# Optimization experiments

Hardware: AMD Instinct MI355X
Metric: run time of the kernel (lower is better)

Reference implementation:

```python
import jax, jax.numpy as jnp
import numpy as np

B, S, HID = 1, 4096, 2048
NH, NKV, HD = 16, 4, 128
BLK, LOCAL, GLOB, STRIDE = 128, 4, 4, 8
NEG = -1e9


def _rotate_half(x):
    x1 = x[..., : x.shape[-1] // 2]
    x2 = x[..., x.shape[-1] // 2 :]
    return jnp.concatenate([-x2, x1], axis=-1)


def setup_inputs() -> dict:
    key = jax.random.key(0)
    ks = jax.random.split(key, 6)
    hidden_states = jax.random.normal(ks[0], (B, S, HID), jnp.float32)
    attention_mask_2d = jnp.ones((B, S), jnp.float32)
    # RoPE tables (b=1 broadcasts over batch, heads)
    pos = jnp.arange(S, dtype=jnp.float32)
    inv = 1.0 / (10000.0 ** (jnp.arange(0, HD, 2, dtype=jnp.float32) / HD))
    fr = pos[:, None] * inv[None, :]
    emb = jnp.concatenate([fr, fr], axis=-1)
    cos = jnp.cos(emb)[None]
    sin = jnp.sin(emb)[None]
    sc = 0.02
    Wq = jax.random.normal(ks[1], (HID, NH * HD), jnp.float32) * sc
    Wk = jax.random.normal(ks[2], (HID, NKV * HD), jnp.float32) * sc
    Wv = jax.random.normal(ks[3], (HID, NKV * HD), jnp.float32) * sc
    Wo = jax.random.normal(ks[4], (NH * HD, HID), jnp.float32) * sc
    return dict(hidden_states=hidden_states, attention_mask_2d=attention_mask_2d,
                cos=cos, sin=sin, Wq=Wq, Wk=Wk, Wv=Wv, Wo=Wo)


def reference(hidden_states, attention_mask_2d, cos, sin, Wq, Wk, Wv, Wo):
    b, Sq, _ = hidden_states.shape
    q = (hidden_states @ Wq).reshape(b, Sq, NH, HD).transpose(0, 2, 1, 3)
    k = (hidden_states @ Wk).reshape(b, Sq, NKV, HD).transpose(0, 2, 1, 3)
    v = (hidden_states @ Wv).reshape(b, Sq, NKV, HD).transpose(0, 2, 1, 3)
    c, s = cos[:, None], sin[:, None]  # broadcast over heads
    q = q * c + _rotate_half(q) * s
    k = k * c + _rotate_half(k) * s
    rep = NH // NKV
    k = jnp.repeat(k, rep, axis=1)
    v = jnp.repeat(v, rep, axis=1)

    scaling = HD ** -0.5
    N = Sq // BLK  # seq divisible by block_size -> pad=0 in the original
    qb = q.reshape(b, NH, N, BLK, HD).astype(jnp.float32)
    kb = k.reshape(b, NH, N, BLK, HD).astype(jnp.float32)
    vb = v.reshape(b, NH, N, BLK, HD).astype(jnp.float32)
    km = attention_mask_2d.reshape(b, N, BLK)

    # ---- local windows: LOCAL blocks ending at the current block ----
    Lp = LOCAL - 1
    kp = jnp.pad(kb, ((0, 0), (0, 0), (Lp, 0), (0, 0), (0, 0)))
    vp = jnp.pad(vb, ((0, 0), (0, 0), (Lp, 0), (0, 0), (0, 0)))
    kmp = jnp.pad(km, ((0, 0), (Lp, 0), (0, 0)))  # padded blocks masked (0)
    win = jnp.arange(N)[:, None] + jnp.arange(LOCAL)[None, :]  # (N, LOCAL)
    k_local = kp[:, :, win]          # (b,h,N,LOCAL,BLK,HD)
    v_local = vp[:, :, win]
    km_local = kmp[:, win]           # (b,N,LOCAL,BLK)

    s_local = jnp.einsum('bhntd,bhnlsd->bhntls', qb, k_local) * scaling
    s_local = s_local + (1.0 - km_local)[:, None, :, None, :, :] * NEG
    intra = jnp.triu(jnp.full((BLK, BLK), NEG, jnp.float32), 1)  # causal inside current block only
    s_local = s_local.at[:, :, :, :, -1, :].add(intra)
    s_local = s_local.reshape(b, NH, N, BLK, LOCAL * BLK)

    # ---- global blocks: block 0 + strided past blocks, dedup -> masked ----
    i = jnp.arange(N)
    offsets = jnp.arange(GLOB - 1, 0, -1) * STRIDE
    idx = jnp.clip(i[:, None] - offsets[None, :], 0)
    idx = jnp.concatenate([jnp.zeros((N, 1), idx.dtype), idx], axis=1)  # (N, GLOB)
    dup = idx[:, 1:] == idx[:, :-1]
    g_valid = jnp.concatenate([jnp.ones((N, 1), bool), ~dup], axis=1).astype(jnp.float32)
    k_g = kb[:, :, idx]              # (b,h,N,GLOB,BLK,HD) gather of global blocks
    v_g = vb[:, :, idx]
    km_g = km[:, idx] * g_valid[None, :, :, None]  # (b,N,GLOB,BLK)

    s_g = jnp.einsum('bhntd,bhngsd->bhntgs', qb, k_g) * scaling
    s_g = s_g + (1.0 - km_g)[:, None, :, None, :, :] * NEG
    s_g = s_g.reshape(b, NH, N, BLK, GLOB * BLK)

    scores = jnp.concatenate([s_local, s_g], axis=-1)  # (b,h,N,BLK,(LOCAL+GLOB)*BLK)
    v_all = jnp.concatenate([v_local.reshape(b, NH, N, LOCAL * BLK, HD),
                             v_g.reshape(b, NH, N, GLOB * BLK, HD)], axis=-2)
    probs = jax.nn.softmax(scores, axis=-1)  # dropout_p = 0 (eval)
    out = jnp.einsum('bhntk,bhnkd->bhntd', probs, v_all)
    out = out.reshape(b, NH, Sq, HD).transpose(0, 2, 1, 3).reshape(b, Sq, NH * HD)
    return out @ Wo
```

## Files before the change

### kernel.cpp

```cpp
#include <hip/hip_runtime.h>
#include <hip/hip_bf16.h>
#include <cstdint>

#define NEGV   (-1000000000.0f)
#define SCALE  0.08838834764831845f

typedef __bf16 bf16x8 __attribute__((ext_vector_type(8)));
typedef float  f32x4  __attribute__((ext_vector_type(4)));
typedef unsigned short u16;
typedef unsigned int   u32;

#define MFMA16(a, b, c) __builtin_amdgcn_mfma_f32_16x16x32_bf16((a), (b), (c), 0, 0, 0)

#define WS_XP    ((size_t)0)
#define WS_AOP   ((size_t)0)
#define WS_WQP   ((size_t)8388608)
#define WS_WKP   ((size_t)12582912)
#define WS_WVP   ((size_t)13631488)
#define WS_WOP   ((size_t)14680064)
#define WS_QF    ((size_t)18874368)
#define WS_KF    ((size_t)27262976)
#define WS_VF    ((size_t)29360128)

__device__ __forceinline__ u16 f2bf(float f) {
  union { float f; u32 u; } v; v.f = f;
  u32 u = v.u;
  u += 0x7FFFu + ((u >> 16) & 1u);
  return (u16)(u >> 16);
}

__device__ __forceinline__ void gl_lds16(const u16* g, u16* l) {
  __builtin_amdgcn_global_load_lds((const __attribute__((address_space(1))) u32*)g,
                                   (__attribute__((address_space(3))) u32*)l,
                                   16, 0, 0);
}

__device__ __forceinline__ int fragoff(int row, int k) {
  return ((row >> 4) * 64 + ((k >> 3) & 3) * 16 + (row & 15)) * 8 + (k & 7);
}

__global__ __launch_bounds__(256, 4)
void convert_kernel(const float* __restrict__ X,
                    const float* __restrict__ Wq,
                    const float* __restrict__ Wk,
                    const float* __restrict__ Wv,
                    const float* __restrict__ Wo,
                    u16* __restrict__ ws)
{
  const int t = blockIdx.x;
  const int tid = threadIdx.x;
  const float* src; u16* dst; int tt, ldn; bool amode = false;
  if (t < 2048)      { src = X;  dst = ws + WS_XP;  tt = t;        ldn = 2048; amode = true; }
  else if (t < 3072) { src = Wq; dst = ws + WS_WQP; tt = t - 2048; ldn = 2048; }
  else if (t < 3328) { src = Wk; dst = ws + WS_WKP; tt = t - 3072; ldn = 512;  }
  else if (t < 3584) { src = Wv; dst = ws + WS_WVP; tt = t - 3328; ldn = 512;  }
  else               { src = Wo; dst = ws + WS_WOP; tt = t - 3584; ldn = 2048; }
  const int rb = tt >> 6, kb = tt & 63;

  if (amode) {
    #pragma unroll
    for (int p = 0; p < 2; ++p) {
      const int c = tid + 256 * p;
      const int row = (c >> 6) * 16 + (c & 15);
      const int k0  = ((c >> 4) & 3) * 8;
      union { u16 h[8]; uint4 v; } pk;
      const float* s0 = src + (size_t)(rb * 128 + row) * 2048 + kb * 32 + k0;
      const float4 a0 = *reinterpret_cast<const float4*>(s0);
      const float4 a1 = *reinterpret_cast<const float4*>(s0 + 4);
      pk.h[0] = f2bf(a0.x); pk.h[1] = f2bf(a0.y); pk.h[2] = f2bf(a0.z); pk.h[3] = f2bf(a0.w);
      pk.h[4] = f2bf(a1.x); pk.h[5] = f2bf(a1.y); pk.h[6] = f2bf(a1.z); pk.h[7] = f2bf(a1.w);
      *reinterpret_cast<uint4*>(dst + (size_t)tt * 4096 + c * 8) = pk.v;
    }
  } else {
    __shared__ u16 Ls[32][136];
    #pragma unroll
    for (int i = 0; i < 4; ++i) {
      const int c = tid + 256 * i;
      const int k = c >> 5, n4 = c & 31;
      const float4 wv = *reinterpret_cast<const float4*>(
          src + (size_t)(kb * 32 + k) * ldn + rb * 128 + n4 * 4);
      u16* d = &Ls[k][n4 * 4];
      d[0] = f2bf(wv.x); d[1] = f2bf(wv.y); d[2] = f2bf(wv.z); d[3] = f2bf(wv.w);
    }
    __syncthreads();
    #pragma unroll
    for (int p = 0; p < 2; ++p) {
      const int c = tid + 256 * p;
      const int row = (c >> 6) * 16 + (c & 15);
      const int k0  = ((c >> 4) & 3) * 8;
      union { u16 h[8]; uint4 v; } pk;
      #pragma unroll
      for (int j = 0; j < 8; ++j) pk.h[j] = Ls[k0 + j][row];
      *reinterpret_cast<uint4*>(dst + (size_t)tt * 4096 + c * 8) = pk.v;
    }
  }
}

__device__ __forceinline__ void gemm_core(const u16* __restrict__ pa,
                                          const u16* __restrict__ pb,
                                          u16* As, u16* Bs,
                                          int tid, int wave, int lane,
                                          f32x4 acc[2][8])
{
  for (int it = 0; it < 64; ++it) {
    __syncthreads();
    gl_lds16(pa + tid * 8,         As + tid * 8);
    gl_lds16(pa + (tid + 256) * 8, As + (tid + 256) * 8);
    gl_lds16(pb + tid * 8,         Bs + tid * 8);
    gl_lds16(pb + (tid + 256) * 8, Bs + (tid + 256) * 8);
    pa += 4096; pb += 4096;
    __syncthreads();
    bf16x8 af0 = *reinterpret_cast<const bf16x8*>(As + (wave * 2 + 0) * 512 + lane * 8);
    bf16x8 af1 = *reinterpret_cast<const bf16x8*>(As + (wave * 2 + 1) * 512 + lane * 8);
    #pragma unroll
    for (int nt = 0; nt < 8; ++nt) {
      const bf16x8 bfr = *reinterpret_cast<const bf16x8*>(Bs + nt * 512 + lane * 8);
      acc[0][nt] = MFMA16(af0, bfr, acc[0][nt]);
      acc[1][nt] = MFMA16(af1, bfr, acc[1][nt]);
    }
  }
}

__global__ __launch_bounds__(256, 2)
void qkv_kernel(const float* __restrict__ cosp,
                const float* __restrict__ sinp,
                u16* __restrict__ ws)
{
  const int mb = blockIdx.x, bn = blockIdx.y;
  const int tid = threadIdx.x;
  const int wave = tid >> 6, lane = tid & 63;
  const int lq = lane >> 4, l16 = lane & 15;

  const u16* Ab = ws + WS_XP + (size_t)mb * 64 * 4096;
  const u16* Bb; int seg, hh;
  if (bn < 16)      { Bb = ws + WS_WQP + (size_t)bn * 64 * 4096;        seg = 0; hh = bn; }
  else if (bn < 20) { Bb = ws + WS_WKP + (size_t)(bn - 16) * 64 * 4096; seg = 1; hh = bn - 16; }
  else              { Bb = ws + WS_WVP + (size_t)(bn - 20) * 64 * 4096; seg = 2; hh = bn - 20; }

  __shared__ __align__(16) u16 As[4096];
  __shared__ __align__(16) u16 Bs[4096];

  f32x4 acc[2][8];
  #pragma unroll
  for (int i = 0; i < 2; ++i)
    #pragma unroll
    for (int j = 0; j < 8; ++j)
      #pragma unroll
      for (int r = 0; r < 4; ++r) acc[i][j][r] = 0.0f;

  gemm_core(Ab, Bb, As, Bs, tid, wave, lane, acc);

  const int m0 = mb * 128;
  if (seg == 2) {
    u16* V = ws + WS_VF + (size_t)hh * 524288;
    #pragma unroll
    for (int mt = 0; mt < 2; ++mt)
      #pragma unroll
      for (int nt = 0; nt < 8; ++nt) {
        const int d = nt * 16 + l16;
        #pragma unroll
        for (int r = 0; r < 4; ++r) {
          const int s = m0 + wave * 32 + mt * 16 + lq * 4 + r;
          V[(s >> 5) * 4096 + fragoff(d, s & 31)] = f2bf(acc[mt][nt][r]);
        }
      }
  } else {
    u16* D = ws + ((seg == 0) ? WS_QF : WS_KF) + (size_t)hh * 524288;
    #pragma unroll
    for (int mt = 0; mt < 2; ++mt)
      #pragma unroll
      for (int r = 0; r < 4; ++r) {
        const int s = m0 + wave * 32 + mt * 16 + lq * 4 + r;
        const int sl = s & 127;
        u16* Dt = D + (size_t)(s >> 7) * 16384;
        #pragma unroll
        for (int nt = 0; nt < 4; ++nt) {
          const int d1 = nt * 16 + l16, d2 = d1 + 64;
          const float c  = cosp[s * 128 + d1];
          const float sn = sinp[s * 128 + d1];
          const float v1 = acc[mt][nt][r], v2 = acc[mt][nt + 4][r];
          Dt[(d1 >> 5) * 4096 + fragoff(sl, d1 & 31)] = f2bf(v1 * c - v2 * sn);
          Dt[(d2 >> 5) * 4096 + fragoff(sl, d2 & 31)] = f2bf(v2 * c + v1 * sn);
        }
      }
  }
}

__global__ __launch_bounds__(512, 4)
void attn_kernel(const float* __restrict__ amask, u16* __restrict__ ws)
{
  const int n = blockIdx.x, h = blockIdx.y;
  const int kvh = h >> 2;
  const int tid = threadIdx.x;
  const int wave = tid >> 6, lane = tid & 63;
  const int lq = lane >> 4, l16 = lane & 15;

  const u16* Kfb = ws + WS_KF + (size_t)kvh * 524288;
  const u16* Vfb = ws + WS_VF + (size_t)kvh * 524288;
  u16* AOp = ws + WS_AOP;

  __shared__ __align__(16) u16 bufK[16384];
  __shared__ __align__(16) u16 bufV[16384];

  const u16* Qb = ws + WS_QF + (size_t)h * 524288 + (size_t)n * 16384;
  bf16x8 qf[4];
  #pragma unroll
  for (int kk = 0; kk < 4; ++kk)
    qf[kk] = *reinterpret_cast<const bf16x8*>(Qb + (size_t)kk * 4096 + (wave * 64 + lane) * 8);

  f32x4 O[8];
  #pragma unroll
  for (int j = 0; j < 8; ++j)
    #pragma unroll
    for (int r = 0; r < 4; ++r) O[j][r] = 0.0f;
  float mrow[4], lrow[4];
  #pragma unroll
  for (int r = 0; r < 4; ++r) { mrow[r] = -3.0e38f; lrow[r] = 0.0f; }

  int gidx[4]; bool gval[4];
  gidx[0] = 0;
  gidx[1] = (n - 24 > 0) ? n - 24 : 0;
  gidx[2] = (n - 16 > 0) ? n - 16 : 0;
  gidx[3] = (n - 8  > 0) ? n - 8  : 0;
  gval[0] = true;
  gval[1] = (gidx[1] != gidx[0]);
  gval[2] = (gidx[2] != gidx[1]);
  gval[3] = (gidx[3] != gidx[2]);

  for (int kb = 0; kb < 8; ++kb) {
    int bkey; bool bvalid; bool intra;
    if (kb < 4) { bkey = n - 3 + kb; bvalid = (bkey >= 0); intra = (kb == 3); }
    else        { bkey = gidx[kb - 4]; bvalid = gval[kb - 4]; intra = false; }
    if (!bvalid) continue;

    const u16* Kb = Kfb + (size_t)bkey * 16384;
    const u16* Vb = Vfb + (size_t)bkey * 16384;
    __syncthreads();
    #pragma unroll
    for (int p = 0; p < 4; ++p) {
      gl_lds16(Kb + (tid + 512 * p) * 8, bufK + (tid + 512 * p) * 8);
      gl_lds16(Vb + (tid + 512 * p) * 8, bufV + (tid + 512 * p) * 8);
    }
    __syncthreads();

    f32x4 sacc[8];
    #pragma unroll
    for (int j = 0; j < 8; ++j)
      #pragma unroll
      for (int r = 0; r < 4; ++r) sacc[j][r] = 0.0f;
    #pragma unroll
    for (int kk = 0; kk < 4; ++kk)
      #pragma unroll
      for (int nt = 0; nt < 8; ++nt) {
        const bf16x8 bfr = *reinterpret_cast<const bf16x8*>(
            bufK + ((kk * 8 + nt) * 64 + lane) * 8);
        sacc[nt] = MFMA16(qf[kk], bfr, sacc[nt]);
      }

    float kmv[8];
    #pragma unroll
    for (int nt = 0; nt < 8; ++nt)
      kmv[nt] = amask[bkey * 128 + nt * 16 + l16];

    __syncthreads();

    u16* pw = bufK + wave * 2048;
    #pragma unroll
    for (int r = 0; r < 4; ++r) {
      const int tq = wave * 16 + lq * 4 + r;
      float sv[8];
      float rmax = -3.0e38f;
      #pragma unroll
      for (int nt = 0; nt < 8; ++nt) {
        float s = sacc[nt][r] * SCALE + (1.0f - kmv[nt]) * NEGV;
        const int tk = nt * 16 + l16;
        if (intra && tk > tq) s += NEGV;
        sv[nt] = s;
        rmax = fmaxf(rmax, s);
      }
      #pragma unroll
      for (int off = 1; off < 16; off <<= 1)
        rmax = fmaxf(rmax, __shfl_xor(rmax, off, 64));
      const float mold = mrow[r];
      const float mnew = fmaxf(mold, rmax);
      const float alpha = __expf(mold - mnew);
      float rsum = 0.0f;
      u16 pb[8];
      #pragma unroll
      for (int nt = 0; nt < 8; ++nt) {
        const float pe = __expf(sv[nt] - mnew);
        rsum += pe;
        pb[nt] = f2bf(pe);
      }
      #pragma unroll
      for (int off = 1; off < 16; off <<= 1)
        rsum += __shfl_xor(rsum, off, 64);
      lrow[r] = lrow[r] * alpha + rsum;
      mrow[r] = mnew;
      #pragma unroll
      for (int nt = 0; nt < 8; ++nt) O[nt][r] *= alpha;
      #pragma unroll
      for (int nt = 0; nt < 8; ++nt)
        pw[(nt >> 1) * 512 + ((((nt & 1) * 2 + (l16 >> 3)) * 16) + lq * 4 + r) * 8 + (l16 & 7)] = pb[nt];
    }

    #pragma unroll
    for (int kk = 0; kk < 4; ++kk) {
      const bf16x8 pf = *reinterpret_cast<const bf16x8*>(pw + kk * 512 + lane * 8);
      #pragma unroll
      for (int nt = 0; nt < 8; ++nt) {
        const bf16x8 vfr = *reinterpret_cast<const bf16x8*>(
            bufV + ((kk * 8 + nt) * 64 + lane) * 8);
        O[nt] = MFMA16(pf, vfr, O[nt]);
      }
    }
  }

  #pragma unroll
  for (int r = 0; r < 4; ++r) {
    const float inv = 1.0f / lrow[r];
    const int s = n * 128 + wave * 16 + lq * 4 + r;
    #pragma unroll
    for (int nt = 0; nt < 8; ++nt) {
      const int kcol = h * 128 + nt * 16 + l16;
      AOp[((size_t)(s >> 7) * 64 + (kcol >> 5)) * 4096 + fragoff(s & 127, kcol & 31)] =
          f2bf(O[nt][r] * inv);
    }
  }
}

__global__ __launch_bounds__(256, 2)
void outproj_kernel(const u16* __restrict__ ws, float* __restrict__ Out)
{
  const int mb = blockIdx.x, bn = blockIdx.y;
  const int tid = threadIdx.x;
  const int wave = tid >> 6, lane = tid & 63;
  const int lq = lane >> 4, l16 = lane & 15;

  const u16* Ab = ws + WS_AOP + (size_t)mb * 64 * 4096;
  const u16* Bb = ws + WS_WOP + (size_t)bn * 64 * 4096;

  __shared__ __align__(16) u16 As[4096];
  __shared__ __align__(16) u16 Bs[4096];

  f32x4 acc[2][8];
  #pragma unroll
  for (int i = 0; i < 2; ++i)
    #pragma unroll
    for (int j = 0; j < 8; ++j)
      #pragma unroll
      for (int r = 0; r < 4; ++r) acc[i][j][r] = 0.0f;

  gemm_core(Ab, Bb, (u16*)As, (u16*)Bs, tid, wave, lane, acc);

  #pragma unroll
  for (int mt = 0; mt < 2; ++mt)
    #pragma unroll
    for (int nt = 0; nt < 8; ++nt) {
      const int ccol = bn * 128 + nt * 16 + l16;
      #pragma unroll
      for (int r = 0; r < 4; ++r) {
        const int s = mb * 128 + wave * 32 + mt * 16 + lq * 4 + r;
        Out[(size_t)s * 2048 + ccol] = acc[mt][nt][r];
      }
    }
}

extern "C" void kernel_launch(void* const* d_in, const int* in_sizes, int n_in,
                              void* d_out, int out_size, void* d_ws, size_t ws_size,
                              hipStream_t stream) {
  const float* X     = (const float*)d_in[0];
  const float* amask = (const float*)d_in[1];
  const float* cosp  = (const float*)d_in[2];
  const float* sinp  = (const float*)d_in[3];
  const float* Wq    = (const float*)d_in[4];
  const float* Wk    = (const float*)d_in[5];
  const float* Wv    = (const float*)d_in[6];
  const float* Wo    = (const float*)d_in[7];
  float* Out = (float*)d_out;
  u16* ws = (u16*)d_ws;

  hipLaunchKernelGGL(convert_kernel, dim3(4608), dim3(256), 0, stream,
                     X, Wq, Wk, Wv, Wo, ws);
  hipLaunchKernelGGL(qkv_kernel, dim3(32, 24), dim3(256), 0, stream,
                     cosp, sinp, ws);
  hipLaunchKernelGGL(attn_kernel, dim3(32, 16), dim3(512), 0, stream,
                     amask, ws);
  hipLaunchKernelGGL(outproj_kernel, dim3(32, 16), dim3(256), 0, stream,
                     ws, Out);
}
```

Measured before the change: 293.0 us.

## Prefetch next K/V block into registers and fold softmax scale into Q

The attention kernel now loads the next key/value block into registers while the current block is computed, staging it to LDS at the start of the next iteration. P gets its own LDS region, which removes one barrier per block. The softmax scale and log2(e) are folded into Q during the QKV epilogue so the kernel can use exp2 directly. The kernel also loops only over the valid block indices, launches as a 1D grid with the heaviest query blocks first, and uses 96KB of dynamic LDS with a lower occupancy bound. In exchange it uses more registers for the prefetch buffers and keeps fewer blocks resident per CU.

Measured after the change: 345.5 us. 1.18x slower.

```diff
diff --git a/kernel.cpp b/kernel.cpp
--- a/kernel.cpp
+++ b/kernel.cpp
@@ -4,6 +4,9 @@
 
 #define NEGV   (-1000000000.0f)
 #define SCALE  0.08838834764831845f
+#define LOG2E  1.4426950408889634f
+#define QSC    (SCALE * LOG2E)
+#define NEGL2  (NEGV * LOG2E)
 
 typedef __bf16 bf16x8 __attribute__((ext_vector_type(8)));
 typedef float  f32x4  __attribute__((ext_vector_type(4)));
@@ -166,6 +169,7 @@
       }
   } else {
     u16* D = ws + ((seg == 0) ? WS_QF : WS_KF) + (size_t)hh * 524288;
+    const float qs = (seg == 0) ? QSC : 1.0f;
     #pragma unroll
     for (int mt = 0; mt < 2; ++mt)
       #pragma unroll
@@ -179,17 +183,22 @@
           const float c  = cosp[s * 128 + d1];
           const float sn = sinp[s * 128 + d1];
           const float v1 = acc[mt][nt][r], v2 = acc[mt][nt + 4][r];
-          Dt[(d1 >> 5) * 4096 + fragoff(sl, d1 & 31)] = f2bf(v1 * c - v2 * sn);
-          Dt[(d2 >> 5) * 4096 + fragoff(sl, d2 & 31)] = f2bf(v2 * c + v1 * sn);
+          Dt[(d1 >> 5) * 4096 + fragoff(sl, d1 & 31)] = f2bf((v1 * c - v2 * sn) * qs);
+          Dt[(d2 >> 5) * 4096 + fragoff(sl, d2 & 31)] = f2bf((v2 * c + v1 * sn) * qs);
         }
       }
   }
 }
 
-__global__ __launch_bounds__(512, 4)
+__global__ __launch_bounds__(512, 2)
 void attn_kernel(const float* __restrict__ amask, u16* __restrict__ ws)
 {
-  const int n = blockIdx.x, h = blockIdx.y;
+  extern __shared__ u16 smem[];
+  u16* bufK = smem;
+  u16* bufV = smem + 16384;
+  const int bx = blockIdx.x;
+  const int n = 31 - (bx >> 4);
+  const int h = bx & 15;
   const int kvh = h >> 2;
   const int tid = threadIdx.x;
   const int wave = tid >> 6, lane = tid & 63;
@@ -198,9 +207,7 @@
   const u16* Kfb = ws + WS_KF + (size_t)kvh * 524288;
   const u16* Vfb = ws + WS_VF + (size_t)kvh * 524288;
   u16* AOp = ws + WS_AOP;
-
-  __shared__ __align__(16) u16 bufK[16384];
-  __shared__ __align__(16) u16 bufV[16384];
+  u16* Pw = smem + 32768 + wave * 2048;
 
   const u16* Qb = ws + WS_QF + (size_t)h * 524288 + (size_t)n * 16384;
   bf16x8 qf[4];
@@ -217,29 +224,52 @@
   #pragma unroll
   for (int r = 0; r < 4; ++r) { mrow[r] = -3.0e38f; lrow[r] = 0.0f; }
 
-  int gidx[4]; bool gval[4];
-  gidx[0] = 0;
-  gidx[1] = (n - 24 > 0) ? n - 24 : 0;
-  gidx[2] = (n - 16 > 0) ? n - 16 : 0;
-  gidx[3] = (n - 8  > 0) ? n - 8  : 0;
-  gval[0] = true;
-  gval[1] = (gidx[1] != gidx[0]);
-  gval[2] = (gidx[2] != gidx[1]);
-  gval[3] = (gidx[3] != gidx[2]);
-
-  for (int kb = 0; kb < 8; ++kb) {
-    int bkey; bool bvalid; bool intra;
-    if (kb < 4) { bkey = n - 3 + kb; bvalid = (bkey >= 0); intra = (kb == 3); }
-    else        { bkey = gidx[kb - 4]; bvalid = gval[kb - 4]; intra = false; }
-    if (!bvalid) continue;
-
-    const u16* Kb = Kfb + (size_t)bkey * 16384;
-    const u16* Vb = Vfb + (size_t)bkey * 16384;
+  const int L = (n < 3 ? n : 3) + 1;
+  const int G = (n >= 25) ? 3 : (n >= 17) ? 2 : (n >= 9) ? 1 : 0;
+  const int nv = L + 1 + G;
+  #define KBOF(i) ((i) < L ? n - L + 1 + (i) : ((i) == L ? 0 : n - 8 * (G - ((i) - L - 1))))
+
+  uint4 pk[4], pv[4]; float biasN[8];
+  {
+    const int b0 = KBOF(0);
+    const u16* Kb = Kfb + (size_t)b0 * 16384;
+    const u16* Vb = Vfb + (size_t)b0 * 16384;
+    #pragma unroll
+    for (int p = 0; p < 4; ++p) {
+      pk[p] = *reinterpret_cast<const uint4*>(Kb + (tid + 512 * p) * 8);
+      pv[p] = *reinterpret_cast<const uint4*>(Vb + (tid + 512 * p) * 8);
+    }
+    #pragma unroll
+    for (int nt = 0; nt < 8; ++nt)
+      biasN[nt] = (1.0f - amask[b0 * 128 + nt * 16 + l16]) * NEGL2;
+  }
+
+  #pragma unroll
+  for (int i = 0; i < 8; ++i) {
+    if (i >= nv) break;
+    const bool intra = (i == L - 1);
+
     __syncthreads();
     #pragma unroll
     for (int p = 0; p < 4; ++p) {
-      gl_lds16(Kb + (tid + 512 * p) * 8, bufK + (tid + 512 * p) * 8);
-      gl_lds16(Vb + (tid + 512 * p) * 8, bufV + (tid + 512 * p) * 8);
+      *reinterpret_cast<uint4*>(bufK + (tid + 512 * p) * 8) = pk[p];
+      *reinterpret_cast<uint4*>(bufV + (tid + 512 * p) * 8) = pv[p];
+    }
+    float biasC[8];
+    #pragma unroll
+    for (int nt = 0; nt < 8; ++nt) biasC[nt] = biasN[nt];
+    if (i + 1 < nv) {
+      const int nb = KBOF(i + 1);
+      const u16* Kb = Kfb + (size_t)nb * 16384;
+      const u16* Vb = Vfb + (size_t)nb * 16384;
+      #pragma unroll
+      for (int p = 0; p < 4; ++p) {
+        pk[p] = *reinterpret_cast<const uint4*>(Kb + (tid + 512 * p) * 8);
+        pv[p] = *reinterpret_cast<const uint4*>(Vb + (tid + 512 * p) * 8);
+      }
+      #pragma unroll
+      for (int nt = 0; nt < 8; ++nt)
+        biasN[nt] = (1.0f - amask[nb * 128 + nt * 16 + l16]) * NEGL2;
     }
     __syncthreads();
 
@@ -257,14 +287,6 @@
         sacc[nt] = MFMA16(qf[kk], bfr, sacc[nt]);
       }
 
-    float kmv[8];
-    #pragma unroll
-    for (int nt = 0; nt < 8; ++nt)
-      kmv[nt] = amask[bkey * 128 + nt * 16 + l16];
-
-    __syncthreads();
-
-    u16* pw = bufK + wave * 2048;
     #pragma unroll
     for (int r = 0; r < 4; ++r) {
       const int tq = wave * 16 + lq * 4 + r;
@@ -272,9 +294,9 @@
       float rmax = -3.0e38f;
       #pragma unroll
       for (int nt = 0; nt < 8; ++nt) {
-        float s = sacc[nt][r] * SCALE + (1.0f - kmv[nt]) * NEGV;
+        float s = sacc[nt][r] + biasC[nt];
         const int tk = nt * 16 + l16;
-        if (intra && tk > tq) s += NEGV;
+        if (intra && tk > tq) s += NEGL2;
         sv[nt] = s;
         rmax = fmaxf(rmax, s);
       }
@@ -283,12 +305,12 @@
         rmax = fmaxf(rmax, __shfl_xor(rmax, off, 64));
       const float mold = mrow[r];
       const float mnew = fmaxf(mold, rmax);
-      const float alpha = __expf(mold - mnew);
+      const float alpha = exp2f(mold - mnew);
       float rsum = 0.0f;
       u16 pb[8];
       #pragma unroll
       for (int nt = 0; nt < 8; ++nt) {
-        const float pe = __expf(sv[nt] - mnew);
+        const float pe = exp2f(sv[nt] - mnew);
         rsum += pe;
         pb[nt] = f2bf(pe);
       }
@@ -301,12 +323,12 @@
       for (int nt = 0; nt < 8; ++nt) O[nt][r] *= alpha;
       #pragma unroll
       for (int nt = 0; nt < 8; ++nt)
-        pw[(nt >> 1) * 512 + ((((nt & 1) * 2 + (l16 >> 3)) * 16) + lq * 4 + r) * 8 + (l16 & 7)] = pb[nt];
+        Pw[(nt >> 1) * 512 + ((((nt & 1) * 2 + (l16 >> 3)) * 16) + lq * 4 + r) * 8 + (l16 & 7)] = pb[nt];
     }
 
     #pragma unroll
     for (int kk = 0; kk < 4; ++kk) {
-      const bf16x8 pf = *reinterpret_cast<const bf16x8*>(pw + kk * 512 + lane * 8);
+      const bf16x8 pf = *reinterpret_cast<const bf16x8*>(Pw + kk * 512 + lane * 8);
       #pragma unroll
       for (int nt = 0; nt < 8; ++nt) {
         const bf16x8 vfr = *reinterpret_cast<const bf16x8*>(
@@ -315,6 +337,7 @@
       }
     }
   }
+  #undef KBOF
 
   #pragma unroll
   for (int r = 0; r < 4; ++r) {
@@ -380,11 +403,16 @@
   float* Out = (float*)d_out;
   u16* ws = (u16*)d_ws;
 
+  static int lds_set = 0;
+  (void)hipFuncSetAttribute((const void*)attn_kernel,
+                            hipFuncAttributeMaxDynamicSharedMemorySize, 98304);
+  (void)lds_set;
+
   hipLaunchKernelGGL(convert_kernel, dim3(4608), dim3(256), 0, stream,
                      X, Wq, Wk, Wv, Wo, ws);
   hipLaunchKernelGGL(qkv_kernel, dim3(32, 24), dim3(256), 0, stream,
                      cosp, sinp, ws);
-  hipLaunchKernelGGL(attn_kernel, dim3(32, 16), dim3(512), 0, stream,
+  hipLaunchKernelGGL(attn_kernel, dim3(512), dim3(512), 98304, stream,
                      amask, ws);
   hipLaunchKernelGGL(outproj_kernel, dim3(32, 16), dim3(256), 0, stream,
                      ws, Out);
```
